# Kernel optimization log

Hardware: AMD Instinct MI355X
Metric: run time of the kernel (lower is better)

Reference implementation:

```python
import jax, jax.numpy as jnp
import numpy as np

LN_EPS = 1e-5

def setup_inputs() -> dict:
    key = jax.random.key(0)
    ks = jax.random.split(key, 6)
    B, L, F, D, S, C = 64, 4096, 28, 128, 64, 10
    return {
        "x": jax.random.normal(ks[0], (B, 1, L, F), dtype=jnp.float32),
        "W_in": jax.random.normal(ks[1], (D, F), dtype=jnp.float32) * 0.05,
        "b_in": jnp.zeros((D,), dtype=jnp.float32),
        "A": jax.random.normal(ks[2], (S, S), dtype=jnp.float32) * 0.01,
        "Bm": jax.random.normal(ks[3], (S, D), dtype=jnp.float32) * 0.01,
        "Cm": jax.random.normal(ks[4], (D, S), dtype=jnp.float32) * 0.01,
        "ln_g": jnp.ones((D,), dtype=jnp.float32),
        "ln_b": jnp.zeros((D,), dtype=jnp.float32),
        "W_fc": jax.random.normal(ks[5], (C, D), dtype=jnp.float32) * 0.05,
        "b_fc": jnp.zeros((C,), dtype=jnp.float32),
    }

def reference(x, W_in, b_in, A, Bm, Cm, ln_g, ln_b, W_fc, b_fc):
    # x: (B, 1, L, 28) -> (B, L, 28)
    x = jnp.squeeze(x, axis=1)
    # input projection: (B, L, D)
    u = jnp.einsum('blf,df->bld', x, W_in) + b_in
    # precompute B @ u_t for all t: (L, B, S)
    Bu = jnp.einsum('bld,sd->lbs', u, Bm)
    Bdim = x.shape[0]
    S = A.shape[0]
    init_state = jnp.zeros((Bdim, S), dtype=x.dtype)

    def step(state, bu_t):
        new_state = state @ A.T + bu_t  # (B, S)
        return new_state, new_state

    _, states = jax.lax.scan(step, init_state, Bu)  # (L, B, S)
    # output projection: (B, L, D)
    y = jnp.einsum('lbs,ds->bld', states, Cm)
    # GELU (exact, matches torch nn.GELU default) then LayerNorm over D
    y = jax.nn.gelu(y, approximate=False)
    mean = jnp.mean(y, axis=-1, keepdims=True)
    var = jnp.var(y, axis=-1, keepdims=True)
    y = (y - mean) * jax.lax.rsqrt(var + LN_EPS) * ln_g + ln_b
    # AdaptiveAvgPool1d(1) over time -> (B, D)
    pooled = jnp.mean(y, axis=1)
    logits = pooled @ W_fc.T + b_fc  # (B, n_classes)
    return logits
```

## Files before the change

### kernel.cpp

```cpp
#include <hip/hip_runtime.h>
#include <math.h>

#define B_SZ 64
#define L_SZ 4096
#define F_SZ 28
#define D_SZ 128
#define S_SZ 64
#define C_SZ 10

#define J_TAPS 8
#define KF 29
#define KP 32
#define CL 256
#define NCH (L_SZ / CL)
#define XROWS (CL + J_TAPS - 1)
#define XS 32

#define SCALE_W 2097152.0f
#define INV_W   (1.0f / 2097152.0f)

#define WS_T_BYTE 32768

typedef _Float16 half8 __attribute__((ext_vector_type(8)));
typedef float    f32x4 __attribute__((ext_vector_type(4)));

__device__ __forceinline__ float dpp_add16(float v) {
    int x = __float_as_int(v);
    v += __int_as_float(__builtin_amdgcn_update_dpp(0, x, 0xB1, 0xF, 0xF, true));
    x = __float_as_int(v);
    v += __int_as_float(__builtin_amdgcn_update_dpp(0, x, 0x4E, 0xF, 0xF, true));
    x = __float_as_int(v);
    v += __int_as_float(__builtin_amdgcn_update_dpp(0, x, 0x141, 0xF, 0xF, true));
    x = __float_as_int(v);
    v += __int_as_float(__builtin_amdgcn_update_dpp(0, x, 0x140, 0xF, 0xF, true));
    return v;
}

__global__ void __launch_bounds__(256)
prep_kernel(const float* __restrict__ Bm,
            const float* __restrict__ W_in,
            const float* __restrict__ b_in,
            const float* __restrict__ A,
            const float* __restrict__ Cm,
            _Float16* __restrict__ Tf16,
            float* __restrict__ pool_ws) {
    __shared__ float A_lds[S_SZ * S_SZ];
    __shared__ float V[J_TAPS][S_SZ];

    const int tid = threadIdx.x;
    const int f = blockIdx.x;

    for (int idx = f * 256 + tid; idx < B_SZ * D_SZ; idx += KF * 256)
        pool_ws[idx] = 0.f;
    if (f < 3)
        for (int idx = tid; idx < J_TAPS * D_SZ; idx += 256)
            Tf16[idx * KP + KF + f] = (_Float16)0.f;

    for (int i = tid * 4; i < S_SZ * S_SZ; i += 1024)
        *(float4*)(A_lds + i) = *(const float4*)(A + i);

    {
        const int s = tid >> 2, dq = tid & 3;
        const float* bm = Bm + s * D_SZ + dq * 32;
        float acc = 0.f;
        if (f < F_SZ) {
            const float* wi = W_in + (dq * 32) * F_SZ + f;
#pragma unroll
            for (int d = 0; d < 32; ++d) acc = fmaf(bm[d], wi[d * F_SZ], acc);
        } else {
            const float* bi = b_in + dq * 32;
#pragma unroll
            for (int d = 0; d < 32; ++d) acc = fmaf(bm[d], bi[d], acc);
        }
        acc += __shfl_xor(acc, 1);
        acc += __shfl_xor(acc, 2);
        if (dq == 0) V[0][s] = acc;
    }
    __syncthreads();

    for (int j = 1; j < J_TAPS; ++j) {
        const int s = tid >> 2, kq = tid & 3;
        const float* ar = A_lds + s * S_SZ + kq * 16;
        const float* vp = V[j - 1] + kq * 16;
        float acc = 0.f;
#pragma unroll
        for (int k = 0; k < 16; ++k) acc = fmaf(ar[k], vp[k], acc);
        acc += __shfl_xor(acc, 1);
        acc += __shfl_xor(acc, 2);
        if (kq == 0) V[j][s] = acc;
        __syncthreads();
    }

    if (tid < D_SZ) {
        const int d = tid;
        float crow[S_SZ];
#pragma unroll
        for (int i = 0; i < 16; ++i) {
            float4 v = *(const float4*)(Cm + d * S_SZ + 4 * i);
            crow[4*i+0] = v.x; crow[4*i+1] = v.y; crow[4*i+2] = v.z; crow[4*i+3] = v.w;
        }
#pragma unroll
        for (int j = 0; j < J_TAPS; ++j) {
            float acc = 0.f;
#pragma unroll
            for (int s = 0; s < S_SZ; ++s) acc = fmaf(crow[s], V[j][s], acc);
            Tf16[(j * D_SZ + d) * KP + f] = (_Float16)(acc * SCALE_W);
        }
    }
}

__global__ void __launch_bounds__(256, 2)
main_kernel(const float* __restrict__ x,
            const _Float16* __restrict__ Tf16,
            float* __restrict__ pool_ws) {
    __shared__ __align__(16) _Float16 xh[XROWS * XS];

    const int tid  = threadIdx.x;
    const int w    = tid >> 6;
    const int col  = tid & 15;
    const int quad = (tid & 63) >> 4;
    const int ch = blockIdx.x;
    const int b  = blockIdx.y;

    {
        const float* xbase = x + ((size_t)b * L_SZ + ch * CL - (J_TAPS - 1)) * F_SZ;
        for (int task = tid; task < XROWS * 4; task += 256) {
            const int rt = task >> 2, g = task & 3;
            half8 h = (half8){0, 0, 0, 0, 0, 0, 0, 0};
            if (!(ch == 0 && rt < J_TAPS - 1)) {
                const float* s0 = xbase + rt * F_SZ + g * 8;
                float4 v0 = *(const float4*)s0;
                h[0] = (_Float16)v0.x; h[1] = (_Float16)v0.y;
                h[2] = (_Float16)v0.z; h[3] = (_Float16)v0.w;
                if (g < 3) {
                    float4 v1 = *(const float4*)(s0 + 4);
                    h[4] = (_Float16)v1.x; h[5] = (_Float16)v1.y;
                    h[6] = (_Float16)v1.z; h[7] = (_Float16)v1.w;
                } else {
                    h[4] = (_Float16)1.f;
                }
            }
            *(half8*)(xh + rt * XS + g * 8) = h;
        }
    }
    __syncthreads();

    f32x4 acc[4][8];
#pragma unroll
    for (int tb = 0; tb < 4; ++tb)
#pragma unroll
        for (int db = 0; db < 8; ++db) acc[tb][db] = (f32x4){0.f, 0.f, 0.f, 0.f};

#pragma unroll
    for (int j = 0; j < J_TAPS; ++j) {
        half8 bfj[8];
#pragma unroll
        for (int db = 0; db < 8; ++db)
            bfj[db] = *(const half8*)(Tf16 + ((j * D_SZ + db * 16 + col) * KP + quad * 8));
#pragma unroll
        for (int tb = 0; tb < 4; ++tb) {
            const int rt = (w * 4 + tb) * 16 + col + (J_TAPS - 1) - j;
            half8 af = *(const half8*)(xh + rt * XS + quad * 8);
            acc[tb][0] = __builtin_amdgcn_mfma_f32_16x16x32_f16(af, bfj[0], acc[tb][0], 0, 0, 0);
            acc[tb][1] = __builtin_amdgcn_mfma_f32_16x16x32_f16(af, bfj[1], acc[tb][1], 0, 0, 0);
            acc[tb][2] = __builtin_amdgcn_mfma_f32_16x16x32_f16(af, bfj[2], acc[tb][2], 0, 0, 0);
            acc[tb][3] = __builtin_amdgcn_mfma_f32_16x16x32_f16(af, bfj[3], acc[tb][3], 0, 0, 0);
            acc[tb][4] = __builtin_amdgcn_mfma_f32_16x16x32_f16(af, bfj[4], acc[tb][4], 0, 0, 0);
            acc[tb][5] = __builtin_amdgcn_mfma_f32_16x16x32_f16(af, bfj[5], acc[tb][5], 0, 0, 0);
            acc[tb][6] = __builtin_amdgcn_mfma_f32_16x16x32_f16(af, bfj[6], acc[tb][6], 0, 0, 0);
            acc[tb][7] = __builtin_amdgcn_mfma_f32_16x16x32_f16(af, bfj[7], acc[tb][7], 0, 0, 0);
        }
    }

#pragma unroll
    for (int tb = 0; tb < 4; ++tb)
#pragma unroll
        for (int db = 0; db < 8; ++db)
#pragma unroll
            for (int r = 0; r < 4; ++r) {
                float y = acc[tb][db][r] * INV_W;
                float y2 = y * y;
                float p = 0.7978845608028654f + y2 * (-0.1329807601338109f
                        + y2 * (0.0199471140200717f - y2 * 0.0023746714184595f));
                float t5 = 0.5f * y;
                acc[tb][db][r] = fmaf(t5 * y, p, t5);
            }

    float pool[8] = {0.f, 0.f, 0.f, 0.f, 0.f, 0.f, 0.f, 0.f};
    float mr = 0.f;
#pragma unroll
    for (int tb = 0; tb < 4; ++tb)
#pragma unroll
        for (int r = 0; r < 4; ++r) {
            float s = 0.f, q = 0.f;
#pragma unroll
            for (int db = 0; db < 8; ++db) {
                float g = acc[tb][db][r];
                s += g; q = fmaf(g, g, q);
            }
            s = dpp_add16(s); q = dpp_add16(q);
            float mean = s * (1.0f / 128.0f);
            float var  = q * (1.0f / 128.0f) - mean * mean;
            float rstd = 1.0f / sqrtf(var + 1e-5f);
            mr = fmaf(mean, rstd, mr);
#pragma unroll
            for (int db = 0; db < 8; ++db)
                pool[db] = fmaf(acc[tb][db][r], rstd, pool[db]);
        }

    __syncthreads();
    float* pp = (float*)xh;
#pragma unroll
    for (int db = 0; db < 8; ++db) {
        float vd = pool[db] - mr;
        vd += __shfl_xor(vd, 16);
        vd += __shfl_xor(vd, 32);
        if (quad == 0) pp[w * D_SZ + db * 16 + col] = vd;
    }
    __syncthreads();
    if (tid < D_SZ)
        atomicAdd(&pool_ws[b * D_SZ + tid],
                  (pp[tid] + pp[D_SZ + tid]) + (pp[2 * D_SZ + tid] + pp[3 * D_SZ + tid]));
}

__global__ void __launch_bounds__(64)
head_kernel(const float* __restrict__ pool_ws,
            const float* __restrict__ ln_g,
            const float* __restrict__ ln_b,
            const float* __restrict__ W_fc,
            const float* __restrict__ b_fc,
            float* __restrict__ out) {
    const int b = blockIdx.x;
    const int lane = threadIdx.x;
    const float inv_l = 1.0f / (float)L_SZ;

    float p0 = fmaf(ln_g[lane] * pool_ws[b * D_SZ + lane], inv_l, ln_b[lane]);
    float p1 = fmaf(ln_g[lane + 64] * pool_ws[b * D_SZ + lane + 64], inv_l, ln_b[lane + 64]);

#pragma unroll
    for (int c = 0; c < C_SZ; ++c) {
        float acc = fmaf(p0, W_fc[c * D_SZ + lane], p1 * W_fc[c * D_SZ + lane + 64]);
#pragma unroll
        for (int m = 1; m < 64; m <<= 1) acc += __shfl_xor(acc, m);
        if (lane == 0) out[b * C_SZ + c] = acc + b_fc[c];
    }
}

extern "C" void kernel_launch(void* const* d_in, const int* in_sizes, int n_in,
                              void* d_out, int out_size, void* d_ws, size_t ws_size,
                              hipStream_t stream) {
    const float* x    = (const float*)d_in[0];
    const float* W_in = (const float*)d_in[1];
    const float* b_in = (const float*)d_in[2];
    const float* A    = (const float*)d_in[3];
    const float* Bm   = (const float*)d_in[4];
    const float* Cm   = (const float*)d_in[5];
    const float* ln_g = (const float*)d_in[6];
    const float* ln_b = (const float*)d_in[7];
    const float* W_fc = (const float*)d_in[8];
    const float* b_fc = (const float*)d_in[9];
    float* out = (float*)d_out;

    float*    pool_ws = (float*)d_ws;
    _Float16* Tf16    = (_Float16*)((char*)d_ws + WS_T_BYTE);

    prep_kernel<<<KF, 256, 0, stream>>>(Bm, W_in, b_in, A, Cm, Tf16, pool_ws);
    main_kernel<<<dim3(NCH, B_SZ), 256, 0, stream>>>(x, Tf16, pool_ws);
    head_kernel<<<B_SZ, 64, 0, stream>>>(pool_ws, ln_g, ln_b, W_fc, b_fc, out);
}
```

Before: 131.8 us.

## Split waves 2x2 over time and D, share LayerNorm stats through LDS

The main kernel's wave tiling changes from four waves each covering 64 time rows by all 128 features to a 2x2 split: two time halves times two 64-wide feature halves. Each wave now loads half as many tap-weight fragments from global memory per tap, but reads twice as many activation fragments from LDS. Because each row's LayerNorm now spans two waves, per-row partial sums and sums of squares go through shared memory, which adds an extra barrier. The GELU polynomial is also refactored into vectorised f32x4 form with pre-scaled coefficients.

```diff
diff --git a/kernel.cpp b/kernel.cpp
--- a/kernel.cpp
+++ b/kernel.cpp
@@ -23,6 +23,7 @@
 
 typedef _Float16 half8 __attribute__((ext_vector_type(8)));
 typedef float    f32x4 __attribute__((ext_vector_type(4)));
+typedef float    f32x2 __attribute__((ext_vector_type(2)));
 
 __device__ __forceinline__ float dpp_add16(float v) {
     int x = __float_as_int(v);
@@ -117,6 +118,8 @@
 
     const int tid  = threadIdx.x;
     const int w    = tid >> 6;
+    const int wt   = w >> 1;
+    const int wd   = w & 1;
     const int col  = tid & 15;
     const int quad = (tid & 63) >> 4;
     const int ch = blockIdx.x;
@@ -145,82 +148,104 @@
     }
     __syncthreads();
 
-    f32x4 acc[4][8];
-#pragma unroll
-    for (int tb = 0; tb < 4; ++tb)
-#pragma unroll
-        for (int db = 0; db < 8; ++db) acc[tb][db] = (f32x4){0.f, 0.f, 0.f, 0.f};
+    f32x4 acc[8][4];
+#pragma unroll
+    for (int tb = 0; tb < 8; ++tb)
+#pragma unroll
+        for (int db = 0; db < 4; ++db) acc[tb][db] = (f32x4){0.f, 0.f, 0.f, 0.f};
+
+    const _Float16* tp = Tf16 + ((wd * 64 + col) * KP + quad * 8);
 
 #pragma unroll
     for (int j = 0; j < J_TAPS; ++j) {
-        half8 bfj[8];
-#pragma unroll
-        for (int db = 0; db < 8; ++db)
-            bfj[db] = *(const half8*)(Tf16 + ((j * D_SZ + db * 16 + col) * KP + quad * 8));
-#pragma unroll
-        for (int tb = 0; tb < 4; ++tb) {
-            const int rt = (w * 4 + tb) * 16 + col + (J_TAPS - 1) - j;
+        half8 bfj[4];
+#pragma unroll
+        for (int db = 0; db < 4; ++db)
+            bfj[db] = *(const half8*)(tp + (j * D_SZ + db * 16) * KP);
+#pragma unroll
+        for (int tb = 0; tb < 8; ++tb) {
+            const int rt = (wt * 8 + tb) * 16 + col + (J_TAPS - 1) - j;
             half8 af = *(const half8*)(xh + rt * XS + quad * 8);
             acc[tb][0] = __builtin_amdgcn_mfma_f32_16x16x32_f16(af, bfj[0], acc[tb][0], 0, 0, 0);
             acc[tb][1] = __builtin_amdgcn_mfma_f32_16x16x32_f16(af, bfj[1], acc[tb][1], 0, 0, 0);
             acc[tb][2] = __builtin_amdgcn_mfma_f32_16x16x32_f16(af, bfj[2], acc[tb][2], 0, 0, 0);
             acc[tb][3] = __builtin_amdgcn_mfma_f32_16x16x32_f16(af, bfj[3], acc[tb][3], 0, 0, 0);
-            acc[tb][4] = __builtin_amdgcn_mfma_f32_16x16x32_f16(af, bfj[4], acc[tb][4], 0, 0, 0);
-            acc[tb][5] = __builtin_amdgcn_mfma_f32_16x16x32_f16(af, bfj[5], acc[tb][5], 0, 0, 0);
-            acc[tb][6] = __builtin_amdgcn_mfma_f32_16x16x32_f16(af, bfj[6], acc[tb][6], 0, 0, 0);
-            acc[tb][7] = __builtin_amdgcn_mfma_f32_16x16x32_f16(af, bfj[7], acc[tb][7], 0, 0, 0);
-        }
-    }
-
-#pragma unroll
-    for (int tb = 0; tb < 4; ++tb)
-#pragma unroll
-        for (int db = 0; db < 8; ++db)
-#pragma unroll
-            for (int r = 0; r < 4; ++r) {
-                float y = acc[tb][db][r] * INV_W;
-                float y2 = y * y;
-                float p = 0.7978845608028654f + y2 * (-0.1329807601338109f
-                        + y2 * (0.0199471140200717f - y2 * 0.0023746714184595f));
-                float t5 = 0.5f * y;
-                acc[tb][db][r] = fmaf(t5 * y, p, t5);
-            }
-
-    float pool[8] = {0.f, 0.f, 0.f, 0.f, 0.f, 0.f, 0.f, 0.f};
+        }
+    }
+
+#pragma unroll
+    for (int tb = 0; tb < 8; ++tb)
+#pragma unroll
+        for (int db = 0; db < 4; ++db) {
+            f32x4 a  = acc[tb][db];
+            f32x4 bb = a * (0.5f * INV_W);
+            f32x4 b2 = bb * bb;
+            f32x4 P  = b2 * (-0.3039579415628160f) + 0.6383076486422944f;
+            P = b2 * P + (-1.0638460810704872f);
+            P = b2 * P + 1.5957691216057308f;
+            acc[tb][db] = b2 * P + bb;
+        }
+
+    float* pls = (float*)xh;
+    __syncthreads();
+#pragma unroll
+    for (int tb = 0; tb < 8; ++tb) {
+        f32x4 g0 = acc[tb][0], g1 = acc[tb][1], g2 = acc[tb][2], g3 = acc[tb][3];
+        f32x4 sv = (g0 + g1) + (g2 + g3);
+        f32x4 qv = g0 * g0;
+        qv = g1 * g1 + qv;
+        qv = g2 * g2 + qv;
+        qv = g3 * g3 + qv;
+        const int tbase = (wt * 8 + tb) * 16 + quad * 4;
+#pragma unroll
+        for (int r = 0; r < 4; ++r) {
+            float s = dpp_add16(sv[r]);
+            float q = dpp_add16(qv[r]);
+            if (col == 0)
+                *(f32x2*)(pls + (tbase + r) * 4 + wd * 2) = (f32x2){s, q};
+        }
+    }
+    __syncthreads();
+
+    f32x4 poolv[4];
+#pragma unroll
+    for (int db = 0; db < 4; ++db) poolv[db] = (f32x4){0.f, 0.f, 0.f, 0.f};
     float mr = 0.f;
 #pragma unroll
-    for (int tb = 0; tb < 4; ++tb)
+    for (int tb = 0; tb < 8; ++tb) {
+        const int tbase = (wt * 8 + tb) * 16 + quad * 4;
+        f32x4 rstd4;
 #pragma unroll
         for (int r = 0; r < 4; ++r) {
-            float s = 0.f, q = 0.f;
-#pragma unroll
-            for (int db = 0; db < 8; ++db) {
-                float g = acc[tb][db][r];
-                s += g; q = fmaf(g, g, q);
-            }
-            s = dpp_add16(s); q = dpp_add16(q);
+            f32x4 pq = *(const f32x4*)(pls + (tbase + r) * 4);
+            float s = pq[0] + pq[2];
+            float q = pq[1] + pq[3];
             float mean = s * (1.0f / 128.0f);
             float var  = q * (1.0f / 128.0f) - mean * mean;
             float rstd = 1.0f / sqrtf(var + 1e-5f);
             mr = fmaf(mean, rstd, mr);
-#pragma unroll
-            for (int db = 0; db < 8; ++db)
-                pool[db] = fmaf(acc[tb][db][r], rstd, pool[db]);
-        }
-
-    __syncthreads();
-    float* pp = (float*)xh;
-#pragma unroll
-    for (int db = 0; db < 8; ++db) {
-        float vd = pool[db] - mr;
+            rstd4[r] = rstd;
+        }
+#pragma unroll
+        for (int db = 0; db < 4; ++db)
+            poolv[db] = poolv[db] + acc[tb][db] * rstd4;
+    }
+
+    float* pp = pls + 1024;
+#pragma unroll
+    for (int db = 0; db < 4; ++db) {
+        float vd = (poolv[db][0] + poolv[db][1]) + (poolv[db][2] + poolv[db][3]);
+        vd -= mr;
         vd += __shfl_xor(vd, 16);
         vd += __shfl_xor(vd, 32);
-        if (quad == 0) pp[w * D_SZ + db * 16 + col] = vd;
-    }
-    __syncthreads();
-    if (tid < D_SZ)
+        if (quad == 0) pp[w * 64 + db * 16 + col] = vd;
+    }
+    __syncthreads();
+    if (tid < D_SZ) {
+        const int dl = tid & 63, dh = tid >> 6;
         atomicAdd(&pool_ws[b * D_SZ + tid],
-                  (pp[tid] + pp[D_SZ + tid]) + (pp[2 * D_SZ + tid] + pp[3 * D_SZ + tid]));
+                  pp[dh * 64 + dl] + pp[(2 + dh) * 64 + dl]);
+    }
 }
 
 __global__ void __launch_bounds__(64)
```

New measurement: 134.5 us. 1.02x slower.
